# Optimization experiments

Measured on AMD Instinct MI355X. Metric: run time of the kernel, lower is better.

## Reference

```python
import jax, jax.numpy as jnp
import numpy as np

EPS = 1e-5

def _layer_norm(x, gamma, beta):
    mu = jnp.mean(x, axis=-1, keepdims=True)
    var = jnp.mean(jnp.square(x - mu), axis=-1, keepdims=True)
    return (x - mu) * jax.lax.rsqrt(var + EPS) * gamma + beta

def setup_inputs() -> dict:
    key = jax.random.key(0)
    ks = jax.random.split(key, 6)
    B, D, H = 8192, 1024, 1024
    x = jax.random.normal(ks[0], (B, D), dtype=jnp.float32)
    h0 = jax.random.normal(ks[1], (B, H), dtype=jnp.float32)
    c0 = jax.random.normal(ks[2], (B, H), dtype=jnp.float32)
    # learned params (orthogonal init approximated by scaled normal for reference purposes)
    weight_h = jax.random.normal(ks[3], (H, 4 * H), dtype=jnp.float32) / np.sqrt(H)
    weight_x = jax.random.normal(ks[4], (D, 4 * H), dtype=jnp.float32) / np.sqrt(D)
    bias = jnp.zeros((4 * H,), dtype=jnp.float32).at[:H].set(1.0)  # forget-gate bias init to 1
    ln1_g = jnp.ones((4 * H,), jnp.float32); ln1_b = jnp.zeros((4 * H,), jnp.float32)
    ln2_g = jnp.ones((4 * H,), jnp.float32); ln2_b = jnp.zeros((4 * H,), jnp.float32)
    ln3_g = jnp.ones((H,), jnp.float32); ln3_b = jnp.zeros((H,), jnp.float32)
    return {"x": x, "h0": h0, "c0": c0, "weight_h": weight_h, "weight_x": weight_x,
            "bias": bias, "ln1_g": ln1_g, "ln1_b": ln1_b, "ln2_g": ln2_g, "ln2_b": ln2_b,
            "ln3_g": ln3_g, "ln3_b": ln3_b}

def reference(x, h0, c0, weight_h, weight_x, bias, ln1_g, ln1_b, ln2_g, ln2_b, ln3_g, ln3_b):
    # gates: [B, 4H] = LN(h0 @ Wh) + LN(x @ Wx) + bias
    gates = _layer_norm(h0 @ weight_h, ln1_g, ln1_b) + _layer_norm(x @ weight_x, ln2_g, ln2_b) + bias
    H = h0.shape[-1]
    f_g, i_g, o_g, c_g = jnp.split(gates, 4, axis=1)  # forget, in, out, cell
    c1 = jax.nn.sigmoid(f_g) * c0 + jax.nn.sigmoid(i_g) * jnp.tanh(c_g)
    h1 = jax.nn.sigmoid(o_g) * jnp.tanh(_layer_norm(c1, ln3_g, ln3_b))
    return (h1, c1)
```

## Files before the change

kernel.cpp:

```cpp
#include <hip/hip_runtime.h>
#include <cstdint>

#define B_ROWS 8192
#define KDIM 1024
#define N4 4096

typedef __attribute__((ext_vector_type(8))) short short8;
typedef __attribute__((ext_vector_type(4))) float float4v;

__device__ __forceinline__ unsigned short f2bf(float f) {
  union { float f; unsigned int u; } v; v.f = f;
  unsigned int r = v.u + 0x7fffu + ((v.u >> 16) & 1u);
  return (unsigned short)(r >> 16);
}

__device__ __forceinline__ float bf2f(unsigned short s) {
  union { unsigned int u; float f; } v; v.u = ((unsigned int)s) << 16;
  return v.f;
}

__device__ __forceinline__ void async16(const unsigned short* g, unsigned short* l) {
  auto gp = (const __attribute__((address_space(1))) unsigned int*)(uintptr_t)g;
  auto lp = (__attribute__((address_space(3))) unsigned int*)(unsigned int)(uintptr_t)l;
  __builtin_amdgcn_global_load_lds(gp, lp, 16, 0, 0);
}

__device__ __forceinline__ float sigm(float v) { return 1.f / (1.f + expf(-v)); }


__global__ __launch_bounds__(256) void cast_bf16(const float* __restrict__ in0,
                                                 unsigned short* __restrict__ out0,
                                                 const float* __restrict__ in1,
                                                 unsigned short* __restrict__ out1) {
  const float* in = blockIdx.y ? in1 : in0;
  unsigned short* out = blockIdx.y ? out1 : out0;
  int i = (blockIdx.x * 256 + threadIdx.x) * 4;
  float4 v = *(const float4*)(in + i);
  ushort4 o;
  o.x = f2bf(v.x); o.y = f2bf(v.y); o.z = f2bf(v.z); o.w = f2bf(v.w);
  *(ushort4*)(out + i) = o;
}

__global__ __launch_bounds__(256) void transpose_cast(const float* __restrict__ W0,
                                                      unsigned short* __restrict__ Wt0,
                                                      const float* __restrict__ W1,
                                                      unsigned short* __restrict__ Wt1) {
  const float* W = blockIdx.z ? W1 : W0;
  unsigned short* Wt = blockIdx.z ? Wt1 : Wt0;
  __shared__ float tile[32][33];
  int n0 = blockIdx.x * 32;
  int k0 = blockIdx.y * 32;
  int tx = threadIdx.x & 31;
  int ty = threadIdx.x >> 5;
#pragma unroll
  for (int i = 0; i < 32; i += 8)
    tile[ty + i][tx] = W[(size_t)(k0 + ty + i) * N4 + n0 + tx];
  __syncthreads();
#pragma unroll
  for (int i = 0; i < 32; i += 8)
    Wt[(size_t)(n0 + ty + i) * KDIM + k0 + tx] = f2bf(tile[tx][ty + i]);
}


__global__ __launch_bounds__(256) void gemm_bf16(
    const unsigned short* __restrict__ Ah, const unsigned short* __restrict__ Wth,
    unsigned short* __restrict__ Uh,
    const unsigned short* __restrict__ Ax, const unsigned short* __restrict__ Wtx,
    unsigned short* __restrict__ Ux, int row0) {
  const unsigned short* A; const unsigned short* W; unsigned short* U;
  if (blockIdx.z == 0) { A = Ah; W = Wth; U = Uh; } else { A = Ax; W = Wtx; U = Ux; }

  __shared__ unsigned short ldsA[128 * 64];
  __shared__ unsigned short ldsB[128 * 64];

  const int tid = threadIdx.x;
  const int wave = tid >> 6;
  const int lane = tid & 63;
  const int wm = (wave & 1) * 64;
  const int wn = (wave >> 1) * 64;

  const int m0 = row0 + blockIdx.y * 128;
  const int n0 = blockIdx.x * 128;

  const int r8 = lane >> 3;
  const int c8 = lane & 7;
  const int g8 = (c8 - r8) & 7;
  const unsigned short* gA0 = A + (size_t)(m0 + wave * 32 + r8) * KDIM + g8 * 8;
  const unsigned short* gB0 = W + (size_t)(n0 + wave * 32 + r8) * KDIM + g8 * 8;
  unsigned short* lA0 = ldsA + (wave * 32) * 64;
  unsigned short* lB0 = ldsB + (wave * 32) * 64;

  const short8* fA[2][4];
  const short8* fB[2][4];
#pragma unroll
  for (int kh = 0; kh < 2; ++kh)
#pragma unroll
    for (int i = 0; i < 4; ++i) {
      int ma = wm + i * 16 + (lane & 15);
      int qa = kh * 4 + (lane >> 4);
      fA[kh][i] = (const short8*)(ldsA + ma * 64 + (((qa + ma) & 7) * 8));
      int nb = wn + i * 16 + (lane & 15);
      int qb = kh * 4 + (lane >> 4);
      fB[kh][i] = (const short8*)(ldsB + nb * 64 + (((qb + nb) & 7) * 8));
    }

  float4v acc[4][4];
  float4v zero = {0.f, 0.f, 0.f, 0.f};
#pragma unroll
  for (int i = 0; i < 4; ++i)
#pragma unroll
    for (int j = 0; j < 4; ++j) acc[i][j] = zero;

  for (int kt = 0; kt < KDIM; kt += 64) {
#pragma unroll
    for (int j = 0; j < 4; ++j) {
      async16(gA0 + kt + j * 8 * KDIM, lA0 + j * 8 * 64);
      async16(gB0 + kt + j * 8 * KDIM, lB0 + j * 8 * 64);
    }
    __syncthreads();
#pragma unroll
    for (int kh = 0; kh < 2; ++kh) {
      short8 a[4], b[4];
#pragma unroll
      for (int i = 0; i < 4; ++i) { a[i] = *fA[kh][i]; b[i] = *fB[kh][i]; }
#pragma unroll
      for (int mi = 0; mi < 4; ++mi)
#pragma unroll
        for (int ni = 0; ni < 4; ++ni)
          acc[mi][ni] = __builtin_amdgcn_mfma_f32_16x16x32_bf16(a[mi], b[ni], acc[mi][ni], 0, 0, 0);
    }
    __syncthreads();
  }

  const int colc = lane & 15;
  const int rowq = (lane >> 4) * 4;
  unsigned short* Ub = U + (size_t)(blockIdx.y * 128 + wm + rowq) * N4 + n0 + wn + colc;
#pragma unroll
  for (int mi = 0; mi < 4; ++mi)
#pragma unroll
    for (int r = 0; r < 4; ++r) {
      unsigned short* Urow = Ub + (size_t)(mi * 16 + r) * N4;
#pragma unroll
      for (int ni = 0; ni < 4; ++ni) Urow[ni * 16] = f2bf(acc[mi][ni][r]);
    }
}


__global__ __launch_bounds__(256) void fused_ln_lstm(
    const unsigned short* __restrict__ Uh, const unsigned short* __restrict__ Ux,
    const float* __restrict__ c0, const float* __restrict__ bias,
    const float* __restrict__ g1, const float* __restrict__ b1,
    const float* __restrict__ g2, const float* __restrict__ b2,
    const float* __restrict__ g3, const float* __restrict__ b3,
    float* __restrict__ h1o, float* __restrict__ c1o, int row0) {
  const int t = threadIdx.x;
  const int lane = t & 63;
  const int wv = t >> 6;
  const size_t rloc = blockIdx.x;
  const size_t rabs = rloc + (size_t)row0;

  const ushort4* uh = (const ushort4*)(Uh + rloc * N4);
  const ushort4* ux = (const ushort4*)(Ux + rloc * N4);
  float4 cold = ((const float4*)(c0 + rabs * KDIM))[t];

  float4 vh[4], vx[4];
  float sh = 0.f, qh = 0.f, sx = 0.f, qx = 0.f;
#pragma unroll
  for (int k = 0; k < 4; ++k) {
    ushort4 au = uh[k * 256 + t];
    float4 a; a.x = bf2f(au.x); a.y = bf2f(au.y); a.z = bf2f(au.z); a.w = bf2f(au.w);
    vh[k] = a;
    sh += (a.x + a.y) + (a.z + a.w);
    qh += a.x * a.x + a.y * a.y + a.z * a.z + a.w * a.w;
    ushort4 bu = ux[k * 256 + t];
    float4 b; b.x = bf2f(bu.x); b.y = bf2f(bu.y); b.z = bf2f(bu.z); b.w = bf2f(bu.w);
    vx[k] = b;
    sx += (b.x + b.y) + (b.z + b.w);
    qx += b.x * b.x + b.y * b.y + b.z * b.z + b.w * b.w;
  }
  __shared__ float red[4][4];
#pragma unroll
  for (int o = 32; o > 0; o >>= 1) {
    sh += __shfl_down(sh, o); qh += __shfl_down(qh, o);
    sx += __shfl_down(sx, o); qx += __shfl_down(qx, o);
  }
  if (lane == 0) { red[wv][0] = sh; red[wv][1] = qh; red[wv][2] = sx; red[wv][3] = qx; }
  __syncthreads();
  sh = red[0][0] + red[1][0] + red[2][0] + red[3][0];
  qh = red[0][1] + red[1][1] + red[2][1] + red[3][1];
  sx = red[0][2] + red[1][2] + red[2][2] + red[3][2];
  qx = red[0][3] + red[1][3] + red[2][3] + red[3][3];
  const float inv4 = 1.f / 4096.f;
  const float muh = sh * inv4, mux = sx * inv4;
  const float rsh = rsqrtf(qh * inv4 - muh * muh + 1e-5f);
  const float rsx = rsqrtf(qx * inv4 - mux * mux + 1e-5f);

  float4 gate[4];
#pragma unroll
  for (int k = 0; k < 4; ++k) {
    int j = k * 256 + t;
    float4 G1 = ((const float4*)g1)[j], B1 = ((const float4*)b1)[j];
    float4 G2 = ((const float4*)g2)[j], B2 = ((const float4*)b2)[j];
    float4 BB = ((const float4*)bias)[j];
    float4 a = vh[k], b = vx[k], r;
    r.x = (a.x - muh) * rsh * G1.x + B1.x + (b.x - mux) * rsx * G2.x + B2.x + BB.x;
    r.y = (a.y - muh) * rsh * G1.y + B1.y + (b.y - mux) * rsx * G2.y + B2.y + BB.y;
    r.z = (a.z - muh) * rsh * G1.z + B1.z + (b.z - mux) * rsx * G2.z + B2.z + BB.z;
    r.w = (a.w - muh) * rsh * G1.w + B1.w + (b.w - mux) * rsx * G2.w + B2.w + BB.w;
    gate[k] = r;
  }
  float4 fg = gate[0], ig = gate[1], og = gate[2], cg = gate[3];
  float4 c1v;
  c1v.x = sigm(fg.x) * cold.x + sigm(ig.x) * tanhf(cg.x);
  c1v.y = sigm(fg.y) * cold.y + sigm(ig.y) * tanhf(cg.y);
  c1v.z = sigm(fg.z) * cold.z + sigm(ig.z) * tanhf(cg.z);
  c1v.w = sigm(fg.w) * cold.w + sigm(ig.w) * tanhf(cg.w);

  float sc = (c1v.x + c1v.y) + (c1v.z + c1v.w);
  float qc = c1v.x * c1v.x + c1v.y * c1v.y + c1v.z * c1v.z + c1v.w * c1v.w;
#pragma unroll
  for (int o = 32; o > 0; o >>= 1) { sc += __shfl_down(sc, o); qc += __shfl_down(qc, o); }
  __syncthreads();
  if (lane == 0) { red[wv][0] = sc; red[wv][1] = qc; }
  __syncthreads();
  sc = red[0][0] + red[1][0] + red[2][0] + red[3][0];
  qc = red[0][1] + red[1][1] + red[2][1] + red[3][1];
  const float invH = 1.f / 1024.f;
  const float muc = sc * invH;
  const float rsc = rsqrtf(qc * invH - muc * muc + 1e-5f);
  float4 G3 = ((const float4*)g3)[t], B3 = ((const float4*)b3)[t];
  float4 h1v;
  h1v.x = sigm(og.x) * tanhf((c1v.x - muc) * rsc * G3.x + B3.x);
  h1v.y = sigm(og.y) * tanhf((c1v.y - muc) * rsc * G3.y + B3.y);
  h1v.z = sigm(og.z) * tanhf((c1v.z - muc) * rsc * G3.z + B3.z);
  h1v.w = sigm(og.w) * tanhf((c1v.w - muc) * rsc * G3.w + B3.w);

  ((float4*)(h1o + rabs * KDIM))[t] = h1v;
  ((float4*)(c1o + rabs * KDIM))[t] = c1v;
}


extern "C" void kernel_launch(void* const* d_in, const int* in_sizes, int n_in,
                              void* d_out, int out_size, void* d_ws, size_t ws_size,
                              hipStream_t stream) {
  const float* x    = (const float*)d_in[0];
  const float* h0   = (const float*)d_in[1];
  const float* c0   = (const float*)d_in[2];
  const float* Wh   = (const float*)d_in[3];
  const float* Wx   = (const float*)d_in[4];
  const float* bias = (const float*)d_in[5];
  const float* g1   = (const float*)d_in[6];
  const float* b1   = (const float*)d_in[7];
  const float* g2   = (const float*)d_in[8];
  const float* b2   = (const float*)d_in[9];
  const float* g3   = (const float*)d_in[10];
  const float* b3   = (const float*)d_in[11];
  float* h1o = (float*)d_out;
  float* c1o = h1o + (size_t)B_ROWS * KDIM;

  unsigned short* Ah  = (unsigned short*)d_ws;
  unsigned short* Ax  = Ah + (size_t)B_ROWS * KDIM;
  unsigned short* Wth = Ax + (size_t)B_ROWS * KDIM;
  unsigned short* Wtx = Wth + (size_t)N4 * KDIM;
  unsigned short* U = Wtx + (size_t)N4 * KDIM;
  size_t used = ((size_t)B_ROWS * KDIM * 2 + (size_t)N4 * KDIM * 2) * sizeof(unsigned short);
  size_t rem = ws_size > used ? ws_size - used : 0;
  int chunk = (int)(rem / ((size_t)2 * N4 * sizeof(unsigned short)));
  chunk &= ~127;
  if (chunk > B_ROWS) chunk = B_ROWS;
  if (chunk < 128) chunk = 128;

  cast_bf16<<<dim3(B_ROWS * KDIM / 1024, 2), 256, 0, stream>>>(h0, Ah, x, Ax);
  transpose_cast<<<dim3(N4 / 32, KDIM / 32, 2), 256, 0, stream>>>(Wh, Wth, Wx, Wtx);

  for (int r0 = 0; r0 < B_ROWS; r0 += chunk) {
    int rows = chunk;
    if (r0 + rows > B_ROWS) rows = B_ROWS - r0;
    unsigned short* Uh = U;
    unsigned short* Ux = U + (size_t)rows * N4;
    gemm_bf16<<<dim3(N4 / 128, rows / 128, 2), 256, 0, stream>>>(Ah, Wth, Uh, Ax, Wtx, Ux, r0);
    fused_ln_lstm<<<rows, 256, 0, stream>>>(Uh, Ux, c0, bias, g1, b1, g2, b2, g3, b3, h1o, c1o, r0);
  }
}
```

Before: 388.3 us.

## Pre-pack B into MFMA fragment layout and double-buffer A tiles in GEMM

```diff
diff --git a/kernel.cpp b/kernel.cpp
--- a/kernel.cpp
+++ b/kernel.cpp
@@ -41,37 +41,34 @@
   *(ushort4*)(out + i) = o;
 }
 
-__global__ __launch_bounds__(256) void transpose_cast(const float* __restrict__ W0,
-                                                      unsigned short* __restrict__ Wt0,
-                                                      const float* __restrict__ W1,
-                                                      unsigned short* __restrict__ Wt1) {
+__global__ __launch_bounds__(256) void pack_b(const float* __restrict__ W0,
+                                              unsigned short* __restrict__ P0,
+                                              const float* __restrict__ W1,
+                                              unsigned short* __restrict__ P1) {
   const float* W = blockIdx.z ? W1 : W0;
-  unsigned short* Wt = blockIdx.z ? Wt1 : Wt0;
-  __shared__ float tile[32][33];
-  int n0 = blockIdx.x * 32;
-  int k0 = blockIdx.y * 32;
-  int tx = threadIdx.x & 31;
-  int ty = threadIdx.x >> 5;
-#pragma unroll
-  for (int i = 0; i < 32; i += 8)
-    tile[ty + i][tx] = W[(size_t)(k0 + ty + i) * N4 + n0 + tx];
-  __syncthreads();
-#pragma unroll
-  for (int i = 0; i < 32; i += 8)
-    Wt[(size_t)(n0 + ty + i) * KDIM + k0 + tx] = f2bf(tile[tx][ty + i]);
+  unsigned short* P = blockIdx.z ? P1 : P0;
+  const int ti = blockIdx.x;
+  const int c  = blockIdx.y * 4 + (threadIdx.x >> 6);
+  const int l  = threadIdx.x & 63;
+  const int n  = ti * 16 + (l & 15);
+  const int k0 = c * 32 + (l >> 4) * 8;
+  unsigned short o[8];
+#pragma unroll
+  for (int j = 0; j < 8; ++j)
+    o[j] = f2bf(W[(size_t)(k0 + j) * N4 + n]);
+  *(short8*)(P + ((size_t)(ti * 32 + c) * 64 + l) * 8) = *(short8*)o;
 }
 
 
 __global__ __launch_bounds__(256) void gemm_bf16(
-    const unsigned short* __restrict__ Ah, const unsigned short* __restrict__ Wth,
+    const unsigned short* __restrict__ Ah, const unsigned short* __restrict__ Bph,
     unsigned short* __restrict__ Uh,
-    const unsigned short* __restrict__ Ax, const unsigned short* __restrict__ Wtx,
+    const unsigned short* __restrict__ Ax, const unsigned short* __restrict__ Bpx,
     unsigned short* __restrict__ Ux, int row0) {
-  const unsigned short* A; const unsigned short* W; unsigned short* U;
-  if (blockIdx.z == 0) { A = Ah; W = Wth; U = Uh; } else { A = Ax; W = Wtx; U = Ux; }
-
-  __shared__ unsigned short ldsA[128 * 64];
-  __shared__ unsigned short ldsB[128 * 64];
+  const unsigned short* A; const unsigned short* Bp; unsigned short* U;
+  if (blockIdx.z == 0) { A = Ah; Bp = Bph; U = Uh; } else { A = Ax; Bp = Bpx; U = Ux; }
+
+  __shared__ unsigned short ldsA[2][128 * 64];
 
   const int tid = threadIdx.x;
   const int wave = tid >> 6;
@@ -86,23 +83,9 @@
   const int c8 = lane & 7;
   const int g8 = (c8 - r8) & 7;
   const unsigned short* gA0 = A + (size_t)(m0 + wave * 32 + r8) * KDIM + g8 * 8;
-  const unsigned short* gB0 = W + (size_t)(n0 + wave * 32 + r8) * KDIM + g8 * 8;
-  unsigned short* lA0 = ldsA + (wave * 32) * 64;
-  unsigned short* lB0 = ldsB + (wave * 32) * 64;
-
-  const short8* fA[2][4];
-  const short8* fB[2][4];
-#pragma unroll
-  for (int kh = 0; kh < 2; ++kh)
-#pragma unroll
-    for (int i = 0; i < 4; ++i) {
-      int ma = wm + i * 16 + (lane & 15);
-      int qa = kh * 4 + (lane >> 4);
-      fA[kh][i] = (const short8*)(ldsA + ma * 64 + (((qa + ma) & 7) * 8));
-      int nb = wn + i * 16 + (lane & 15);
-      int qb = kh * 4 + (lane >> 4);
-      fB[kh][i] = (const short8*)(ldsB + nb * 64 + (((qb + nb) & 7) * 8));
-    }
+  const int lA0 = (wave * 32) * 64;
+
+  const unsigned short* bBase = Bp + (size_t)((n0 + wn) >> 4) * 16384 + (size_t)lane * 8;
 
   float4v acc[4][4];
   float4v zero = {0.f, 0.f, 0.f, 0.f};
@@ -111,25 +94,61 @@
 #pragma unroll
     for (int j = 0; j < 4; ++j) acc[i][j] = zero;
 
-  for (int kt = 0; kt < KDIM; kt += 64) {
-#pragma unroll
-    for (int j = 0; j < 4; ++j) {
-      async16(gA0 + kt + j * 8 * KDIM, lA0 + j * 8 * 64);
-      async16(gB0 + kt + j * 8 * KDIM, lB0 + j * 8 * 64);
+  short8 b0[2][4], b1[2][4];
+
+#define DMA_A(kt, buf)                                                         \
+  {                                                                            \
+    _Pragma("unroll")                                                          \
+    for (int j = 0; j < 4; ++j)                                                \
+      async16(gA0 + (kt) * 64 + j * 8 * KDIM, &ldsA[buf][lA0 + j * 8 * 64]);   \
+  }
+
+#define LOAD_B(kt, breg)                                                       \
+  {                                                                            \
+    _Pragma("unroll")                                                          \
+    for (int kh = 0; kh < 2; ++kh) {                                           \
+      const int c = (kt) * 2 + kh;                                             \
+      _Pragma("unroll")                                                        \
+      for (int i = 0; i < 4; ++i)                                              \
+        breg[kh][i] = *(const short8*)(bBase + i * 16384 + c * 512);           \
+    }                                                                          \
+  }
+
+#define COMPUTE(buf, breg)                                                     \
+  {                                                                            \
+    _Pragma("unroll")                                                          \
+    for (int kh = 0; kh < 2; ++kh) {                                           \
+      short8 a[4];                                                             \
+      _Pragma("unroll")                                                        \
+      for (int i = 0; i < 4; ++i) {                                            \
+        const int ma = wm + i * 16 + (lane & 15);                              \
+        const int q = kh * 4 + (lane >> 4);                                    \
+        a[i] = *(const short8*)(&ldsA[buf][ma * 64 + ((q + ma) & 7) * 8]);     \
+      }                                                                        \
+      _Pragma("unroll")                                                        \
+      for (int mi = 0; mi < 4; ++mi)                                           \
+        _Pragma("unroll")                                                      \
+        for (int ni = 0; ni < 4; ++ni)                                         \
+          acc[mi][ni] = __builtin_amdgcn_mfma_f32_16x16x32_bf16(               \
+              a[mi], breg[kh][ni], acc[mi][ni], 0, 0, 0);                      \
+    }                                                                          \
+  }
+
+  DMA_A(0, 0);
+  LOAD_B(0, b0);
+
+  for (int p = 0; p < 8; ++p) {
+    const int t0 = 2 * p;
+    __syncthreads();
+    DMA_A(t0 + 1, 1);
+    LOAD_B(t0 + 1, b1);
+    COMPUTE(0, b0);
+    __syncthreads();
+    if (p != 7) {
+      DMA_A(t0 + 2, 0);
+      LOAD_B(t0 + 2, b0);
     }
-    __syncthreads();
-#pragma unroll
-    for (int kh = 0; kh < 2; ++kh) {
-      short8 a[4], b[4];
-#pragma unroll
-      for (int i = 0; i < 4; ++i) { a[i] = *fA[kh][i]; b[i] = *fB[kh][i]; }
-#pragma unroll
-      for (int mi = 0; mi < 4; ++mi)
-#pragma unroll
-        for (int ni = 0; ni < 4; ++ni)
-          acc[mi][ni] = __builtin_amdgcn_mfma_f32_16x16x32_bf16(a[mi], b[ni], acc[mi][ni], 0, 0, 0);
-    }
-    __syncthreads();
+    COMPUTE(1, b1);
   }
 
   const int colc = lane & 15;
@@ -143,6 +162,9 @@
 #pragma unroll
       for (int ni = 0; ni < 4; ++ni) Urow[ni * 16] = f2bf(acc[mi][ni][r]);
     }
+#undef DMA_A
+#undef LOAD_B
+#undef COMPUTE
 }
 
 
@@ -260,9 +282,9 @@
 
   unsigned short* Ah  = (unsigned short*)d_ws;
   unsigned short* Ax  = Ah + (size_t)B_ROWS * KDIM;
-  unsigned short* Wth = Ax + (size_t)B_ROWS * KDIM;
-  unsigned short* Wtx = Wth + (size_t)N4 * KDIM;
-  unsigned short* U = Wtx + (size_t)N4 * KDIM;
+  unsigned short* Bph = Ax + (size_t)B_ROWS * KDIM;
+  unsigned short* Bpx = Bph + (size_t)N4 * KDIM;
+  unsigned short* U = Bpx + (size_t)N4 * KDIM;
   size_t used = ((size_t)B_ROWS * KDIM * 2 + (size_t)N4 * KDIM * 2) * sizeof(unsigned short);
   size_t rem = ws_size > used ? ws_size - used : 0;
   int chunk = (int)(rem / ((size_t)2 * N4 * sizeof(unsigned short)));
@@ -271,14 +293,14 @@
   if (chunk < 128) chunk = 128;
 
   cast_bf16<<<dim3(B_ROWS * KDIM / 1024, 2), 256, 0, stream>>>(h0, Ah, x, Ax);
-  transpose_cast<<<dim3(N4 / 32, KDIM / 32, 2), 256, 0, stream>>>(Wh, Wth, Wx, Wtx);
+  pack_b<<<dim3(N4 / 16, 8, 2), 256, 0, stream>>>(Wh, Bph, Wx, Bpx);
 
   for (int r0 = 0; r0 < B_ROWS; r0 += chunk) {
     int rows = chunk;
     if (r0 + rows > B_ROWS) rows = B_ROWS - r0;
     unsigned short* Uh = U;
     unsigned short* Ux = U + (size_t)rows * N4;
-    gemm_bf16<<<dim3(N4 / 128, rows / 128, 2), 256, 0, stream>>>(Ah, Wth, Uh, Ax, Wtx, Ux, r0);
+    gemm_bf16<<<dim3(N4 / 128, rows / 128, 2), 256, 0, stream>>>(Ah, Bph, Uh, Ax, Bpx, Ux, r0);
     fused_ln_lstm<<<rows, 256, 0, stream>>>(Uh, Ux, c0, bias, g1, b1, g2, b2, g3, b3, h1o, c1o, r0);
   }
 }
```

Measured after the change: 389.5 us. About the same (+0.3%).
